# Optimization experiments

Hardware: AMD Instinct MI355X
Metric: run time of the kernel (lower is better)

## Reference

```python
import jax, jax.numpy as jnp
import numpy as np
from jax import lax

B, H, W = 1024, 28, 28
STEPS, KMAX = 32, 2
OUT_F, NUM_CLASSES = 32, 10
P = H * W  # 784 flattened filtration values
TSEQ1 = jnp.linspace(0.01, 0.29, STEPS, dtype=jnp.float32)
TSEQ2 = jnp.linspace(0.05, 0.3, STEPS, dtype=jnp.float32)
DN = ('NHWC', 'HWIO', 'NHWC')


def setup_inputs() -> dict:
    key = jax.random.key(0)
    ks = jax.random.split(key, 16)
    return {
        'x': jax.random.normal(ks[0], (B, H, W, 1), jnp.float32),
        'x_dtm005': jax.random.uniform(ks[1], (B, H, W, 1), jnp.float32, 0.0, 0.3),
        'x_dtm02': jax.random.uniform(ks[2], (B, H, W, 1), jnp.float32, 0.0, 0.3),
        'conv_w1': jax.random.normal(ks[3], (3, 3, 1, 32), jnp.float32) * 0.1,
        'conv_b1': jnp.zeros((32,), jnp.float32),
        'conv_w2': jax.random.normal(ks[4], (3, 3, 32, 1), jnp.float32) * 0.1,
        'conv_b2': jnp.zeros((1,), jnp.float32),
        'g1_w': jax.random.normal(ks[5], (KMAX * STEPS, OUT_F), jnp.float32) * 0.1,
        'g1_b': jnp.zeros((OUT_F,), jnp.float32),
        'g2_w': jax.random.normal(ks[6], (KMAX * STEPS, OUT_F), jnp.float32) * 0.1,
        'g2_b': jnp.zeros((OUT_F,), jnp.float32),
        'fc1_w': jax.random.normal(ks[7], (P + 2 * OUT_F, 64), jnp.float32) * 0.05,
        'fc1_b': jnp.zeros((64,), jnp.float32),
        'fc2_w': jax.random.normal(ks[8], (64, NUM_CLASSES), jnp.float32) * 0.1,
        'fc2_b': jnp.zeros((NUM_CLASSES,), jnp.float32),
    }


def _landscape(v, tseq):
    """Persistence landscape over a grid of t-values.

    v: [B, P] filtration (DTM) values; each value is a birth time, paired
    with a per-sample death at the max filtration value (sublevel sweep).
    Landscape lambda_k(t) = k-th largest tent max(0, min(t-b, d-t)).
    Returns [B, KMAX*STEPS].
    """
    death = jnp.max(v, axis=1)                                     # [B]
    # tent: [B, T, P]
    tent = jnp.maximum(0.0, jnp.minimum(tseq[None, :, None] - v[:, None, :],
                                        death[:, None, None] - tseq[None, :, None]))
    top = lax.top_k(tent, KMAX)[0]                                 # [B, T, K]
    return jnp.transpose(top, (0, 2, 1)).reshape(v.shape[0], KMAX * tseq.shape[0])


def reference(x, x_dtm005, x_dtm02, conv_w1, conv_b1, conv_w2, conv_b2,
              g1_w, g1_b, g2_w, g2_b, fc1_w, fc1_b, fc2_w, fc2_b):
    b = x.shape[0]
    # TDA branch 1 (sublevel=True -> no negation)
    x1 = _landscape(x_dtm005.reshape(b, -1), TSEQ1)
    x1 = jax.nn.relu(x1 @ g1_w + g1_b)
    # TDA branch 2
    x2 = _landscape(x_dtm02.reshape(b, -1), TSEQ2)
    x2 = jax.nn.relu(x2 @ g2_w + g2_b)
    # CNN branch: Conv(32) -> ReLU -> Conv(1), then extra ReLU per call()
    h = lax.conv_general_dilated(x, conv_w1, (1, 1), 'SAME', dimension_numbers=DN) + conv_b1
    h = jax.nn.relu(h)
    h = lax.conv_general_dilated(h, conv_w2, (1, 1), 'SAME', dimension_numbers=DN) + conv_b2
    h = jax.nn.relu(h)
    hf = h.reshape(b, -1)                                          # [B, 784]
    z = jnp.concatenate([hf, x1, x2], axis=-1)                     # [B, 848]
    z = jax.nn.relu(z @ fc1_w + fc1_b)
    return z @ fc2_w + fc2_b                                       # [B, 10]
```

## Files before the change

kernel.cpp:

```cpp
#include <hip/hip_runtime.h>

#define BATCH 1024
#define PP 784

__global__ __launch_bounds__(256) void convtda_kernel(
    const float* __restrict__ xin,
    const float* __restrict__ w1g, const float* __restrict__ b1g,
    const float* __restrict__ w2g, const float* __restrict__ b2g,
    const float* __restrict__ dtm1, const float* __restrict__ dtm2,
    const float* __restrict__ g1w, const float* __restrict__ g1b,
    const float* __restrict__ g2w, const float* __restrict__ g2b,
    float* __restrict__ hf, float* __restrict__ x12)
{
  const int tid = threadIdx.x;

  if (blockIdx.x >= BATCH) {
    const int b = blockIdx.x - BATCH;
    __shared__ float red[2][4][3];
    __shared__ float fin[2][3];

    for (int br = 0; br < 2; ++br) {
      const float* v = (br == 0 ? dtm1 : dtm2) + b * PP;
      float m1 = 1e30f, m2 = 1e30f, mx = -1e30f;
      for (int i = tid; i < 196; i += 256) {
        float4 x4 = *(const float4*)&v[i * 4];
        float xs[4] = {x4.x, x4.y, x4.z, x4.w};
#pragma unroll
        for (int k = 0; k < 4; ++k) {
          float x = xs[k];
          mx = fmaxf(mx, x);
          float nm1 = fminf(m1, x);
          m2 = fminf(m2, fmaxf(m1, x));
          m1 = nm1;
        }
      }
#pragma unroll
      for (int off = 32; off >= 1; off >>= 1) {
        float o1 = __shfl_xor(m1, off);
        float o2 = __shfl_xor(m2, off);
        float ox = __shfl_xor(mx, off);
        mx = fmaxf(mx, ox);
        float nm1 = fminf(m1, o1);
        m2 = fminf(fminf(m2, o2), fmaxf(m1, o1));
        m1 = nm1;
      }
      if ((tid & 63) == 0) {
        int wid = tid >> 6;
        red[br][wid][0] = m1; red[br][wid][1] = m2; red[br][wid][2] = mx;
      }
    }
    __syncthreads();
    if (tid < 2) {
      float m1 = 1e30f, m2 = 1e30f, mx = -1e30f;
#pragma unroll
      for (int w = 0; w < 4; ++w) {
        float o1 = red[tid][w][0], o2 = red[tid][w][1], ox = red[tid][w][2];
        mx = fmaxf(mx, ox);
        float nm1 = fminf(m1, o1);
        m2 = fminf(fminf(m2, o2), fmaxf(m1, o1));
        m1 = nm1;
      }
      fin[tid][0] = m1; fin[tid][1] = m2; fin[tid][2] = mx;
    }
    __syncthreads();
    if (tid < 64) {
      const int br = tid >> 5, j = tid & 31;
      const float m1 = fin[br][0], m2 = fin[br][1], mx = fin[br][2];
      const float* gw = br ? g2w : g1w;
      const float* gb = br ? g2b : g1b;
      const float t0 = br ? 0.05f : 0.01f;
      const float dt = br ? (0.25f / 31.0f) : (0.28f / 31.0f);
      float acc = gb[j];
#pragma unroll 4
      for (int i = 0; i < 64; ++i) {
        const int k = i >> 5, ti = i & 31;
        float tv = t0 + dt * (float)ti;
        float vk = k ? m2 : m1;
        float lam = fmaxf(0.0f, fminf(tv - vk, mx - tv));
        acc = fmaf(lam, gw[i * 32 + j], acc);
      }
      x12[b * 64 + br * 32 + j] = fmaxf(acc, 0.0f);
    }
    return;
  }

  const int b = blockIdx.x;
  const int lane = tid & 63;
  const int w = tid >> 6;
  const int x = lane & 31;
  const int sub = lane >> 5;

  __shared__ float inL[28][36];
  __shared__ float w1L[9][32];
  __shared__ float w2L[9][32];
  __shared__ float b1L[32];
  __shared__ float pL[4][28][28];

  for (int i = tid; i < 224; i += 256) {
    int y = i >> 3, k = i & 7;
    inL[y][k == 0 ? 0 : 28 + k] = 0.f;
  }
  for (int i = tid; i < 784; i += 256)
    inL[i / 28][i % 28 + 1] = xin[b * PP + i];
  for (int i = tid; i < 288; i += 256) {
    ((float*)w1L)[i] = w1g[i];
    ((float*)w2L)[i] = w2g[i];
  }
  if (tid < 32) b1L[tid] = b1g[tid];
  __syncthreads();

  float acc[28];
#pragma unroll
  for (int y = 0; y < 28; ++y) acc[y] = 0.f;

#pragma unroll 1
  for (int cp = 0; cp < 4; ++cp) {
    const int c = (w << 3) + (cp << 1) + sub;
    float wa[9], wb[9];
#pragma unroll
    for (int t = 0; t < 9; ++t) { wa[t] = w1L[t][c]; wb[t] = w2L[t][c]; }
    const float bb = b1L[c];

    float ra0 = 0.f, ra1 = 0.f, ra2 = 0.f;
    float rb0 = inL[0][x], rb1 = inL[0][x + 1], rb2 = inL[0][x + 2];

#pragma unroll
    for (int y = 0; y < 28; ++y) {
      float rc0, rc1, rc2;
      if (y + 1 < 28) {
        rc0 = inL[y + 1][x]; rc1 = inL[y + 1][x + 1]; rc2 = inL[y + 1][x + 2];
      } else {
        rc0 = 0.f; rc1 = 0.f; rc2 = 0.f;
      }
      float h = bb;
      h = fmaf(ra0, wa[0], h); h = fmaf(ra1, wa[1], h); h = fmaf(ra2, wa[2], h);
      h = fmaf(rb0, wa[3], h); h = fmaf(rb1, wa[4], h); h = fmaf(rb2, wa[5], h);
      h = fmaf(rc0, wa[6], h); h = fmaf(rc1, wa[7], h); h = fmaf(rc2, wa[8], h);
      h = (x < 28) ? fmaxf(h, 0.f) : 0.f;
      float hl = __shfl_up(h, 1, 32);  hl = (x == 0) ? 0.f : hl;
      float hr = __shfl_down(h, 1, 32);
      if (y + 1 < 28) {
        acc[y + 1] = fmaf(hl, wb[0], acc[y + 1]);
        acc[y + 1] = fmaf(h , wb[1], acc[y + 1]);
        acc[y + 1] = fmaf(hr, wb[2], acc[y + 1]);
      }
      acc[y] = fmaf(hl, wb[3], acc[y]);
      acc[y] = fmaf(h , wb[4], acc[y]);
      acc[y] = fmaf(hr, wb[5], acc[y]);
      if (y > 0) {
        acc[y - 1] = fmaf(hl, wb[6], acc[y - 1]);
        acc[y - 1] = fmaf(h , wb[7], acc[y - 1]);
        acc[y - 1] = fmaf(hr, wb[8], acc[y - 1]);
      }
      ra0 = rb0; ra1 = rb1; ra2 = rb2;
      rb0 = rc0; rb1 = rc1; rb2 = rc2;
    }
  }

#pragma unroll
  for (int y = 0; y < 28; ++y) acc[y] += __shfl_xor(acc[y], 32);
  if (sub == 0 && x < 28) {
#pragma unroll
    for (int y = 0; y < 28; ++y) pL[w][y][x] = acc[y];
  }
  __syncthreads();

  const float b2v = b2g[0];
  const float* pw = (const float*)pL;
  for (int u = tid; u < 784; u += 256) {
    float v = pw[u] + pw[784 + u] + pw[1568 + u] + pw[2352 + u] + b2v;
    hf[b * PP + u] = fmaxf(v, 0.f);
  }
}

__global__ __launch_bounds__(256) void fc_kernel(
    const float* __restrict__ hf, const float* __restrict__ x12,
    const float* __restrict__ w1, const float* __restrict__ b1,
    const float* __restrict__ w2, const float* __restrict__ b2,
    float* __restrict__ out)
{
  __shared__ __align__(16) float zL[4][864];
  __shared__ float pL[4][4][64];
  __shared__ float z1L[4][64];
  const int blk = blockIdx.x, tid = threadIdx.x;
  const int s0 = blk * 4;

  for (int i = tid; i < 848; i += 256) {
    int s = i / 212, q = i % 212;
    if (q < 196)
      *(float4*)&zL[s][q * 4] = *(const float4*)&hf[(s0 + s) * 784 + q * 4];
    else
      *(float4*)&zL[s][784 + (q - 196) * 4] =
          *(const float4*)&x12[(s0 + s) * 64 + (q - 196) * 4];
  }
  __syncthreads();

  const int j = tid & 63, part = tid >> 6;
  float acc0 = 0.f, acc1 = 0.f, acc2 = 0.f, acc3 = 0.f;
  const int i0 = part * 212;
#pragma unroll 2
  for (int i = i0; i < i0 + 212; i += 4) {
    float4 z0 = *(float4*)&zL[0][i];
    float4 z1 = *(float4*)&zL[1][i];
    float4 z2 = *(float4*)&zL[2][i];
    float4 z3 = *(float4*)&zL[3][i];
    float wA = w1[(i + 0) * 64 + j];
    float wB = w1[(i + 1) * 64 + j];
    float wC = w1[(i + 2) * 64 + j];
    float wD = w1[(i + 3) * 64 + j];
    acc0 = fmaf(z0.x, wA, acc0); acc0 = fmaf(z0.y, wB, acc0);
    acc0 = fmaf(z0.z, wC, acc0); acc0 = fmaf(z0.w, wD, acc0);
    acc1 = fmaf(z1.x, wA, acc1); acc1 = fmaf(z1.y, wB, acc1);
    acc1 = fmaf(z1.z, wC, acc1); acc1 = fmaf(z1.w, wD, acc1);
    acc2 = fmaf(z2.x, wA, acc2); acc2 = fmaf(z2.y, wB, acc2);
    acc2 = fmaf(z2.z, wC, acc2); acc2 = fmaf(z2.w, wD, acc2);
    acc3 = fmaf(z3.x, wA, acc3); acc3 = fmaf(z3.y, wB, acc3);
    acc3 = fmaf(z3.z, wC, acc3); acc3 = fmaf(z3.w, wD, acc3);
  }
  pL[part][0][j] = acc0; pL[part][1][j] = acc1;
  pL[part][2][j] = acc2; pL[part][3][j] = acc3;
  __syncthreads();
  {
    int s = tid >> 6, jj = tid & 63;
    float v = pL[0][s][jj] + pL[1][s][jj] + pL[2][s][jj] + pL[3][s][jj] + b1[jj];
    z1L[s][jj] = fmaxf(v, 0.f);
  }
  __syncthreads();
  if (tid < 40) {
    int s = tid / 10, o = tid % 10;
    float acc = b2[o];
#pragma unroll 8
    for (int jj = 0; jj < 64; ++jj)
      acc = fmaf(z1L[s][jj], w2[jj * 10 + o], acc);
    out[(s0 + s) * 10 + o] = acc;
  }
}

extern "C" void kernel_launch(void* const* d_in, const int* in_sizes, int n_in,
                              void* d_out, int out_size, void* d_ws, size_t ws_size,
                              hipStream_t stream) {
  const float* x       = (const float*)d_in[0];
  const float* dtm005  = (const float*)d_in[1];
  const float* dtm02   = (const float*)d_in[2];
  const float* conv_w1 = (const float*)d_in[3];
  const float* conv_b1 = (const float*)d_in[4];
  const float* conv_w2 = (const float*)d_in[5];
  const float* conv_b2 = (const float*)d_in[6];
  const float* g1_w    = (const float*)d_in[7];
  const float* g1_b    = (const float*)d_in[8];
  const float* g2_w    = (const float*)d_in[9];
  const float* g2_b    = (const float*)d_in[10];
  const float* fc1_w   = (const float*)d_in[11];
  const float* fc1_b   = (const float*)d_in[12];
  const float* fc2_w   = (const float*)d_in[13];
  const float* fc2_b   = (const float*)d_in[14];
  float* out = (float*)d_out;

  float* hfW  = (float*)d_ws;
  float* x12W = hfW + BATCH * PP;

  convtda_kernel<<<2 * BATCH, 256, 0, stream>>>(
      x, conv_w1, conv_b1, conv_w2, conv_b2,
      dtm005, dtm02, g1_w, g1_b, g2_w, g2_b, hfW, x12W);
  fc_kernel<<<BATCH / 4, 256, 0, stream>>>(hfW, x12W, fc1_w, fc1_b, fc2_w, fc2_b, out);
}
```

Measured before the change: 130.1 us.

## Fuse conv, TDA landscape, and FC layers into one per-sample kernel

Merges the conv/TDA kernel and the FC kernel into a single kernel with one block per sample. The conv output and landscape features stay in shared memory, so the workspace round-trip and the second launch go away. The DTM loads are issued early to overlap with the conv. In exchange, fc1 weights are now read once per sample instead of once per 4 samples, which raises L2 traffic (about 217KB per block). Shared memory per block also grows.

```diff
diff --git a/kernel.cpp b/kernel.cpp
--- a/kernel.cpp
+++ b/kernel.cpp
@@ -3,88 +3,19 @@
 #define BATCH 1024
 #define PP 784
 
-__global__ __launch_bounds__(256) void convtda_kernel(
+__global__ __launch_bounds__(256) void fused_kernel(
     const float* __restrict__ xin,
+    const float* __restrict__ dtm1, const float* __restrict__ dtm2,
     const float* __restrict__ w1g, const float* __restrict__ b1g,
     const float* __restrict__ w2g, const float* __restrict__ b2g,
-    const float* __restrict__ dtm1, const float* __restrict__ dtm2,
     const float* __restrict__ g1w, const float* __restrict__ g1b,
     const float* __restrict__ g2w, const float* __restrict__ g2b,
-    float* __restrict__ hf, float* __restrict__ x12)
+    const float* __restrict__ fc1w, const float* __restrict__ fc1b,
+    const float* __restrict__ fc2w, const float* __restrict__ fc2b,
+    float* __restrict__ out)
 {
+  const int b = blockIdx.x;
   const int tid = threadIdx.x;
-
-  if (blockIdx.x >= BATCH) {
-    const int b = blockIdx.x - BATCH;
-    __shared__ float red[2][4][3];
-    __shared__ float fin[2][3];
-
-    for (int br = 0; br < 2; ++br) {
-      const float* v = (br == 0 ? dtm1 : dtm2) + b * PP;
-      float m1 = 1e30f, m2 = 1e30f, mx = -1e30f;
-      for (int i = tid; i < 196; i += 256) {
-        float4 x4 = *(const float4*)&v[i * 4];
-        float xs[4] = {x4.x, x4.y, x4.z, x4.w};
-#pragma unroll
-        for (int k = 0; k < 4; ++k) {
-          float x = xs[k];
-          mx = fmaxf(mx, x);
-          float nm1 = fminf(m1, x);
-          m2 = fminf(m2, fmaxf(m1, x));
-          m1 = nm1;
-        }
-      }
-#pragma unroll
-      for (int off = 32; off >= 1; off >>= 1) {
-        float o1 = __shfl_xor(m1, off);
-        float o2 = __shfl_xor(m2, off);
-        float ox = __shfl_xor(mx, off);
-        mx = fmaxf(mx, ox);
-        float nm1 = fminf(m1, o1);
-        m2 = fminf(fminf(m2, o2), fmaxf(m1, o1));
-        m1 = nm1;
-      }
-      if ((tid & 63) == 0) {
-        int wid = tid >> 6;
-        red[br][wid][0] = m1; red[br][wid][1] = m2; red[br][wid][2] = mx;
-      }
-    }
-    __syncthreads();
-    if (tid < 2) {
-      float m1 = 1e30f, m2 = 1e30f, mx = -1e30f;
-#pragma unroll
-      for (int w = 0; w < 4; ++w) {
-        float o1 = red[tid][w][0], o2 = red[tid][w][1], ox = red[tid][w][2];
-        mx = fmaxf(mx, ox);
-        float nm1 = fminf(m1, o1);
-        m2 = fminf(fminf(m2, o2), fmaxf(m1, o1));
-        m1 = nm1;
-      }
-      fin[tid][0] = m1; fin[tid][1] = m2; fin[tid][2] = mx;
-    }
-    __syncthreads();
-    if (tid < 64) {
-      const int br = tid >> 5, j = tid & 31;
-      const float m1 = fin[br][0], m2 = fin[br][1], mx = fin[br][2];
-      const float* gw = br ? g2w : g1w;
-      const float* gb = br ? g2b : g1b;
-      const float t0 = br ? 0.05f : 0.01f;
-      const float dt = br ? (0.25f / 31.0f) : (0.28f / 31.0f);
-      float acc = gb[j];
-#pragma unroll 4
-      for (int i = 0; i < 64; ++i) {
-        const int k = i >> 5, ti = i & 31;
-        float tv = t0 + dt * (float)ti;
-        float vk = k ? m2 : m1;
-        float lam = fmaxf(0.0f, fminf(tv - vk, mx - tv));
-        acc = fmaf(lam, gw[i * 32 + j], acc);
-      }
-      x12[b * 64 + br * 32 + j] = fmaxf(acc, 0.0f);
-    }
-    return;
-  }
-
-  const int b = blockIdx.x;
   const int lane = tid & 63;
   const int w = tid >> 6;
   const int x = lane & 31;
@@ -95,6 +26,17 @@
   __shared__ float w2L[9][32];
   __shared__ float b1L[32];
   __shared__ float pL[4][28][28];
+  __shared__ __align__(16) float zL[864];
+  __shared__ float red[2][4][3];
+  __shared__ float fin[2][3];
+  __shared__ float pfc[4][64];
+  __shared__ float z1L[64];
+
+  float4 tv1, tv2;
+  if (tid < 196) {
+    tv1 = *(const float4*)&dtm1[b * PP + tid * 4];
+    tv2 = *(const float4*)&dtm2[b * PP + tid * 4];
+  }
 
   for (int i = tid; i < 224; i += 256) {
     int y = i >> 3, k = i & 7;
@@ -156,7 +98,6 @@
       rb0 = rc0; rb1 = rc1; rb2 = rc2;
     }
   }
-
 #pragma unroll
   for (int y = 0; y < 28; ++y) acc[y] += __shfl_xor(acc[y], 32);
   if (sub == 0 && x < 28) {
@@ -165,74 +106,103 @@
   }
   __syncthreads();
 
-  const float b2v = b2g[0];
-  const float* pw = (const float*)pL;
-  for (int u = tid; u < 784; u += 256) {
-    float v = pw[u] + pw[784 + u] + pw[1568 + u] + pw[2352 + u] + b2v;
-    hf[b * PP + u] = fmaxf(v, 0.f);
-  }
-}
-
-__global__ __launch_bounds__(256) void fc_kernel(
-    const float* __restrict__ hf, const float* __restrict__ x12,
-    const float* __restrict__ w1, const float* __restrict__ b1,
-    const float* __restrict__ w2, const float* __restrict__ b2,
-    float* __restrict__ out)
-{
-  __shared__ __align__(16) float zL[4][864];
-  __shared__ float pL[4][4][64];
-  __shared__ float z1L[4][64];
-  const int blk = blockIdx.x, tid = threadIdx.x;
-  const int s0 = blk * 4;
-
-  for (int i = tid; i < 848; i += 256) {
-    int s = i / 212, q = i % 212;
-    if (q < 196)
-      *(float4*)&zL[s][q * 4] = *(const float4*)&hf[(s0 + s) * 784 + q * 4];
-    else
-      *(float4*)&zL[s][784 + (q - 196) * 4] =
-          *(const float4*)&x12[(s0 + s) * 64 + (q - 196) * 4];
-  }
-  __syncthreads();
-
-  const int j = tid & 63, part = tid >> 6;
-  float acc0 = 0.f, acc1 = 0.f, acc2 = 0.f, acc3 = 0.f;
-  const int i0 = part * 212;
-#pragma unroll 2
-  for (int i = i0; i < i0 + 212; i += 4) {
-    float4 z0 = *(float4*)&zL[0][i];
-    float4 z1 = *(float4*)&zL[1][i];
-    float4 z2 = *(float4*)&zL[2][i];
-    float4 z3 = *(float4*)&zL[3][i];
-    float wA = w1[(i + 0) * 64 + j];
-    float wB = w1[(i + 1) * 64 + j];
-    float wC = w1[(i + 2) * 64 + j];
-    float wD = w1[(i + 3) * 64 + j];
-    acc0 = fmaf(z0.x, wA, acc0); acc0 = fmaf(z0.y, wB, acc0);
-    acc0 = fmaf(z0.z, wC, acc0); acc0 = fmaf(z0.w, wD, acc0);
-    acc1 = fmaf(z1.x, wA, acc1); acc1 = fmaf(z1.y, wB, acc1);
-    acc1 = fmaf(z1.z, wC, acc1); acc1 = fmaf(z1.w, wD, acc1);
-    acc2 = fmaf(z2.x, wA, acc2); acc2 = fmaf(z2.y, wB, acc2);
-    acc2 = fmaf(z2.z, wC, acc2); acc2 = fmaf(z2.w, wD, acc2);
-    acc3 = fmaf(z3.x, wA, acc3); acc3 = fmaf(z3.y, wB, acc3);
-    acc3 = fmaf(z3.z, wC, acc3); acc3 = fmaf(z3.w, wD, acc3);
-  }
-  pL[part][0][j] = acc0; pL[part][1][j] = acc1;
-  pL[part][2][j] = acc2; pL[part][3][j] = acc3;
-  __syncthreads();
   {
-    int s = tid >> 6, jj = tid & 63;
-    float v = pL[0][s][jj] + pL[1][s][jj] + pL[2][s][jj] + pL[3][s][jj] + b1[jj];
-    z1L[s][jj] = fmaxf(v, 0.f);
-  }
-  __syncthreads();
-  if (tid < 40) {
-    int s = tid / 10, o = tid % 10;
-    float acc = b2[o];
+    const float b2v = b2g[0];
+    const float* pw = (const float*)pL;
+    for (int u = tid; u < 784; u += 256) {
+      float v = pw[u] + pw[784 + u] + pw[1568 + u] + pw[2352 + u] + b2v;
+      zL[u] = fmaxf(v, 0.f);
+    }
+  }
+#pragma unroll
+  for (int br = 0; br < 2; ++br) {
+    float m1 = 1e30f, m2 = 1e30f, mx = -1e30f;
+    if (tid < 196) {
+      float4 x4 = br ? tv2 : tv1;
+      float xs[4] = {x4.x, x4.y, x4.z, x4.w};
+#pragma unroll
+      for (int k = 0; k < 4; ++k) {
+        float v = xs[k];
+        mx = fmaxf(mx, v);
+        float nm1 = fminf(m1, v);
+        m2 = fminf(m2, fmaxf(m1, v));
+        m1 = nm1;
+      }
+    }
+#pragma unroll
+    for (int off = 32; off >= 1; off >>= 1) {
+      float o1 = __shfl_xor(m1, off);
+      float o2 = __shfl_xor(m2, off);
+      float ox = __shfl_xor(mx, off);
+      mx = fmaxf(mx, ox);
+      float nm1 = fminf(m1, o1);
+      m2 = fminf(fminf(m2, o2), fmaxf(m1, o1));
+      m1 = nm1;
+    }
+    if ((tid & 63) == 0) {
+      red[br][w][0] = m1; red[br][w][1] = m2; red[br][w][2] = mx;
+    }
+  }
+  __syncthreads();
+  if (tid < 2) {
+    float m1 = 1e30f, m2 = 1e30f, mx = -1e30f;
+#pragma unroll
+    for (int wv = 0; wv < 4; ++wv) {
+      float o1 = red[tid][wv][0], o2 = red[tid][wv][1], ox = red[tid][wv][2];
+      mx = fmaxf(mx, ox);
+      float nm1 = fminf(m1, o1);
+      m2 = fminf(fminf(m2, o2), fmaxf(m1, o1));
+      m1 = nm1;
+    }
+    fin[tid][0] = m1; fin[tid][1] = m2; fin[tid][2] = mx;
+  }
+  __syncthreads();
+  if (tid < 64) {
+    const int br = tid >> 5, j = tid & 31;
+    const float m1 = fin[br][0], m2 = fin[br][1], mx = fin[br][2];
+    const float* gw = br ? g2w : g1w;
+    const float* gb = br ? g2b : g1b;
+    const float t0 = br ? 0.05f : 0.01f;
+    const float dt = br ? (0.25f / 31.0f) : (0.28f / 31.0f);
+    float a = gb[j];
+#pragma unroll 4
+    for (int i = 0; i < 64; ++i) {
+      const int k = i >> 5, ti = i & 31;
+      float tv = t0 + dt * (float)ti;
+      float vk = k ? m2 : m1;
+      float lam = fmaxf(0.0f, fminf(tv - vk, mx - tv));
+      a = fmaf(lam, gw[i * 32 + j], a);
+    }
+    zL[784 + br * 32 + j] = fmaxf(a, 0.0f);
+  }
+  __syncthreads();
+
+  {
+    const int j = tid & 63, part = tid >> 6;
+    float a = 0.f;
+    const int i0 = part * 212;
+#pragma unroll 4
+    for (int i = i0; i < i0 + 212; i += 4) {
+      float4 z4 = *(float4*)&zL[i];
+      a = fmaf(z4.x, fc1w[(i + 0) * 64 + j], a);
+      a = fmaf(z4.y, fc1w[(i + 1) * 64 + j], a);
+      a = fmaf(z4.z, fc1w[(i + 2) * 64 + j], a);
+      a = fmaf(z4.w, fc1w[(i + 3) * 64 + j], a);
+    }
+    pfc[part][j] = a;
+  }
+  __syncthreads();
+  if (tid < 64) {
+    float v = pfc[0][tid] + pfc[1][tid] + pfc[2][tid] + pfc[3][tid] + fc1b[tid];
+    z1L[tid] = fmaxf(v, 0.f);
+  }
+  __syncthreads();
+  if (tid < 10) {
+    float a = fc2b[tid];
 #pragma unroll 8
     for (int jj = 0; jj < 64; ++jj)
-      acc = fmaf(z1L[s][jj], w2[jj * 10 + o], acc);
-    out[(s0 + s) * 10 + o] = acc;
+      a = fmaf(z1L[jj], fc2w[jj * 10 + tid], a);
+    out[b * 10 + tid] = a;
   }
 }
 
@@ -256,11 +226,7 @@
   const float* fc2_b   = (const float*)d_in[14];
   float* out = (float*)d_out;
 
-  float* hfW  = (float*)d_ws;
-  float* x12W = hfW + BATCH * PP;
-
-  convtda_kernel<<<2 * BATCH, 256, 0, stream>>>(
-      x, conv_w1, conv_b1, conv_w2, conv_b2,
-      dtm005, dtm02, g1_w, g1_b, g2_w, g2_b, hfW, x12W);
-  fc_kernel<<<BATCH / 4, 256, 0, stream>>>(hfW, x12W, fc1_w, fc1_b, fc2_w, fc2_b, out);
+  fused_kernel<<<BATCH, 256, 0, stream>>>(
+      x, dtm005, dtm02, conv_w1, conv_b1, conv_w2, conv_b2,
+      g1_w, g1_b, g2_w, g2_b, fc1_w, fc1_b, fc2_w, fc2_b, out);
 }
```

Result: no change. 128.5 us (-1.2%).
